# Kernel optimization log

Hardware: AMD Instinct MI355X
Metric: run time of the kernel (lower is better)

## Reference

```python
import jax, jax.numpy as jnp
import numpy as np

KS = 3          # kernel_size
NK = KS * KS    # sample points per output pixel
PAD = KS // 2   # 'same' zero padding


def setup_inputs() -> dict:
    key = jax.random.key(0)
    k1, k2, k3, k4 = jax.random.split(key, 4)
    B, H, W, C, F = 8, 64, 64, 128, 256
    x = jax.random.normal(k1, (B, H, W, C), jnp.float32)
    offset = jax.random.normal(k2, (B, H, W, 2 * NK), jnp.float32)
    modulation = jax.random.uniform(k3, (B, H, W, NK), jnp.float32)
    conv_kernel = jax.random.normal(k4, (KS, KS, C, F), jnp.float32) * 0.02
    conv_bias = jnp.zeros((F,), jnp.float32)
    return {"x": x, "offset": offset, "modulation": modulation,
            "conv_kernel": conv_kernel, "conv_bias": conv_bias}


def reference(x, offset, modulation, conv_kernel, conv_bias):
    B, H, W, C = x.shape
    # zero pad ('same')
    xp = jnp.pad(x, ((0, 0), (PAD, PAD), (PAD, PAD), (0, 0)))
    ih, iw = H + 2 * PAD, W + 2 * PAD

    # offset: first NK channels are y-offsets, last NK are x-offsets -> [B,H,W,NK,2]
    off = jnp.stack([offset[..., :NK], offset[..., NK:]], axis=-1)

    # pixel centers in padded coords (start at 1 due to padding), stride 1
    gy, gx = jnp.meshgrid(jnp.arange(1, H + 1), jnp.arange(1, W + 1), indexing="ij")
    pix = jnp.stack([gy, gx], -1).reshape(1, H, W, 1, 2).astype(x.dtype)

    # kernel tap offsets, ky varies slowest after flatten (matches TF source)
    ky, kx = jnp.meshgrid(jnp.arange(-PAD, KS - PAD), jnp.arange(-PAD, KS - PAD), indexing="ij")
    ker = jnp.stack([ky.reshape(-1), kx.reshape(-1)], -1).reshape(1, 1, 1, NK, 2).astype(x.dtype)

    p = off + pix + ker                       # [B,H,W,NK,2] sampling locations
    y0f = jnp.floor(p[..., 0])
    x0f = jnp.floor(p[..., 1])
    y0 = jnp.clip(y0f, 0, ih - 1)
    x0 = jnp.clip(x0f, 0, iw - 1)
    y1 = jnp.clip(y0f + 1.0, 0, ih - 1)
    x1 = jnp.clip(x0f + 1.0, 0, iw - 1)

    bidx = jnp.arange(B).reshape(B, 1, 1, 1)

    def gather(yi, xi):  # -> [B,H,W,NK,C]
        return xp[bidx, yi.astype(jnp.int32), xi.astype(jnp.int32)]

    f00 = gather(y0, x0)
    f01 = gather(y1, x0)
    f10 = gather(y0, x1)
    f11 = gather(y1, x1)

    py = jnp.clip(p[..., 0], 0, ih - 1)[..., None]
    px = jnp.clip(p[..., 1], 0, iw - 1)[..., None]
    ly = py - y0[..., None]
    lx = px - x0[..., None]

    feats = ((1.0 - ly) * (1.0 - lx) * f00 + (1.0 - ly) * lx * f01
             + ly * (1.0 - lx) * f10 + ly * lx * f11)      # [B,H,W,NK,C]
    feats = feats * modulation[..., None]

    # rearrange exactly as the TF code: concat kernel-row chunks along H, then reshape
    feats = jnp.concatenate([feats[:, :, :, s:s + KS, :] for s in range(0, NK, KS)], axis=1)
    feats = feats.reshape(B, H * KS, W * KS, C)

    out = jax.lax.conv_general_dilated(
        feats, conv_kernel, window_strides=(KS, KS), padding="VALID",
        dimension_numbers=("NHWC", "HWIO", "NHWC"))
    return out + conv_bias
```

## Files before the change

### kernel.cpp

```cpp
#include <hip/hip_runtime.h>

typedef __attribute__((ext_vector_type(8))) short short8;
typedef __attribute__((ext_vector_type(4))) float f32x4;

__device__ __forceinline__ unsigned short f2bf(float f) {
  union { float f; unsigned u; } v; v.f = f;
  unsigned r = v.u + 0x7FFFu + ((v.u >> 16) & 1u);
  return (unsigned short)(r >> 16);
}

__device__ __forceinline__ short8 pack8(f32x4 a, f32x4 b) {
  short8 p;
  p[0] = (short)f2bf(a.x); p[1] = (short)f2bf(a.y);
  p[2] = (short)f2bf(a.z); p[3] = (short)f2bf(a.w);
  p[4] = (short)f2bf(b.x); p[5] = (short)f2bf(b.y);
  p[6] = (short)f2bf(b.z); p[7] = (short)f2bf(b.w);
  return p;
}

__device__ __forceinline__ short8 packEO(f32x4 e, f32x4 o) {
  short8 p;
  p[0] = (short)f2bf(e.x); p[1] = (short)f2bf(o.x);
  p[2] = (short)f2bf(e.y); p[3] = (short)f2bf(o.y);
  p[4] = (short)f2bf(e.z); p[5] = (short)f2bf(o.z);
  p[6] = (short)f2bf(e.w); p[7] = (short)f2bf(o.w);
  return p;
}

constexpr int KKt = 1152;
constexpr int Ff  = 256;
constexpr size_t WT_BYTES = (size_t)KKt * Ff * 2;
constexpr size_t XB_BYTES = (size_t)8 * 64 * 64 * 128 * 2;

__global__ void wt_prep(const float* __restrict__ kf, unsigned short* __restrict__ wtB) {
  int idx = blockIdx.x * 256 + threadIdx.x;
  int j  = idx & 7;
  int fr = (idx >> 3) & 15;
  int kg = (idx >> 7) & 3;
  int ft = (idx >> 9) & 15;
  int ks = (idx >> 13) & 3;
  int ch = idx >> 15;
  int k = ch * 128 + ks * 32 + kg * 8 + j;
  int f = ft * 16 + fr;
  wtB[idx] = f2bf(kf[k * Ff + f]);
}

__global__ void x_prep(const float* __restrict__ x, unsigned short* __restrict__ xb) {
  int i = (blockIdx.x * 512 + threadIdx.x) * 8;
  const f32x4* p = (const f32x4*)(x + i);
  *(short8*)(xb + i) = pack8(p[0], p[1]);
}

__global__ __launch_bounds__(1024, 8) void dcn_bf16(
    const unsigned short* __restrict__ xb, const float* __restrict__ off,
    const float* __restrict__ mo, const unsigned short* __restrict__ wtB,
    const float* __restrict__ bias, float* __restrict__ out) {
  __shared__ __align__(16) char At[2][64 * 272];

  const int b  = blockIdx.x & 7;
  const int oh = blockIdx.x >> 3;
  const int t  = threadIdx.x;
  const int lane = t & 63;
  const int wv   = t >> 6;
  const int mh   = wv & 1;
  const int fq   = wv >> 1;
  const int fr   = lane & 15;
  const int kg   = lane >> 4;
  const int sow  = t >> 4;
  const int c8   = t & 15;

  f32x4 acc[2][2];
#pragma unroll
  for (int i = 0; i < 2; ++i) { acc[i][0] = f32x4{0,0,0,0}; acc[i][1] = f32x4{0,0,0,0}; }

  float oyr[2], oxr[2], mmr[2];
  int   og[4]; float wg[4];

  auto loadOff = [&](int ch, int sl) {
    const int dy = ch / 3, dxk = ch - dy * 3;
    const int r = 3 * oh + dy, hp = r & 63, kp = ((r >> 6) * 3) + dxk;
    const int pix = (b * 64 + hp) * 64 + sow;
    oyr[sl] = off[pix * 18 + kp];
    oxr[sl] = off[pix * 18 + 9 + kp];
    mmr[sl] = mo[pix * 9 + kp];
  };

  auto calcW = [&](int ch, int sl) {
    const int dy = ch / 3, dxk = ch - dy * 3;
    const int r = 3 * oh + dy, hp = r & 63, kp = ((r >> 6) * 3) + dxk;
    const float py = oyr[sl] + (float)(hp + kp / 3);
    const float px = oxr[sl] + (float)(sow + kp % 3);
    const float mm = mmr[sl];
    const float y0f = floorf(py), x0f = floorf(px);
    const float y0 = fminf(fmaxf(y0f, 0.f), 65.f);
    const float y1 = fminf(fmaxf(y0f + 1.f, 0.f), 65.f);
    const float x0 = fminf(fmaxf(x0f, 0.f), 65.f);
    const float x1 = fminf(fmaxf(x0f + 1.f, 0.f), 65.f);
    const float ly = fminf(fmaxf(py, 0.f), 65.f) - y0;
    const float lx = fminf(fmaxf(px, 0.f), 65.f) - x0;
    wg[0] = (1.f - ly) * (1.f - lx) * mm;
    wg[1] = (1.f - ly) * lx * mm;
    wg[2] = ly * (1.f - lx) * mm;
    wg[3] = ly * lx * mm;
    const int iy0 = (int)y0, iy1 = (int)y1, ix0 = (int)x0, ix1 = (int)x1;
    const int yy[4] = {iy0, iy1, iy0, iy1};
    const int xx[4] = {ix0, ix0, ix1, ix1};
#pragma unroll
    for (int j = 0; j < 4; ++j) {
      const bool v = (yy[j] >= 1) & (yy[j] <= 64) & (xx[j] >= 1) & (xx[j] <= 64);
      int o = ((b * 64 + yy[j] - 1) * 64 + (xx[j] - 1)) * 128 + c8 * 8;
      if (!v) { o = 0; wg[j] = 0.f; }
      og[j] = o;
    }
  };

  auto ldQ = [&](int c) -> short8 {
    return *(const short8*)(xb + og[c]);
  };
  auto accQ = [&](short8 s, float w, f32x4& Pe, f32x4& Po) {
    union { short8 s; unsigned u[4]; } v; v.s = s;
#pragma unroll
    for (int i = 0; i < 4; ++i) {
      union { unsigned u; float f; } e, o;
      e.u = v.u[i] << 16;
      o.u = v.u[i] & 0xffff0000u;
      Pe[i] = fmaf(w, e.f, Pe[i]);
      Po[i] = fmaf(w, o.f, Po[i]);
    }
  };

  auto mmah = [&](int buf, int ch, int ks) {
    const unsigned short* bp = wtB + (((ch * 4 + ks) * 16 + fq * 2) * 64 + lane) * 8;
    short8 bf0 = *(const short8*)bp;
    short8 bf1 = *(const short8*)(bp + 512);
    short8 af[2];
#pragma unroll
    for (int m2 = 0; m2 < 2; ++m2)
      af[m2] = *(const short8*)(At[buf] + (mh * 32 + m2 * 16 + fr) * 272 + ks * 64 + kg * 16);
#pragma unroll
    for (int m2 = 0; m2 < 2; ++m2) {
      acc[m2][0] = __builtin_amdgcn_mfma_f32_16x16x32_bf16(af[m2], bf0, acc[m2][0], 0, 0, 0);
      acc[m2][1] = __builtin_amdgcn_mfma_f32_16x16x32_bf16(af[m2], bf1, acc[m2][1], 0, 0, 0);
    }
  };

  const int wb = sow * 272 + c8 * 16;

  loadOff(0, 0); loadOff(1, 1);
  calcW(0, 0);
  {
    short8 q0 = ldQ(0), q1 = ldQ(1), q2 = ldQ(2), q3 = ldQ(3);
    f32x4 Pe{0,0,0,0}, Po{0,0,0,0};
    accQ(q0, wg[0], Pe, Po); accQ(q1, wg[1], Pe, Po);
    accQ(q2, wg[2], Pe, Po); accQ(q3, wg[3], Pe, Po);
    *(short8*)(At[0] + wb) = packEO(Pe, Po);
  }
  __syncthreads();

#pragma unroll
  for (int ch = 0; ch < 9; ++ch) {
    const int buf = ch & 1;
    const bool hv = ch < 8;
    short8 q0, q1, q2, q3;
    f32x4 Pe{0,0,0,0}, Po{0,0,0,0};
    if (hv) {
      calcW(ch + 1, (ch + 1) & 1);
      q0 = ldQ(0); q1 = ldQ(1);
    }
    mmah(buf, ch, 0);
    if (hv) {
      q2 = ldQ(2); q3 = ldQ(3);
      accQ(q0, wg[0], Pe, Po);
    }
    mmah(buf, ch, 1);
    if (hv) accQ(q1, wg[1], Pe, Po);
    if (ch < 7) loadOff(ch + 2, ch & 1);
    mmah(buf, ch, 2);
    if (hv) {
      accQ(q2, wg[2], Pe, Po);
      accQ(q3, wg[3], Pe, Po);
      *(short8*)(At[buf ^ 1] + wb) = packEO(Pe, Po);
    }
    mmah(buf, ch, 3);
    __syncthreads();
  }

  float bs[2];
#pragma unroll
  for (int nb = 0; nb < 2; ++nb) bs[nb] = bias[fq * 32 + nb * 16 + fr];
  float* orow = out + (long)(b * 64 + oh) * 64 * 256;
#pragma unroll
  for (int m2 = 0; m2 < 2; ++m2) {
#pragma unroll
    for (int j = 0; j < 4; ++j) {
      const int row = mh * 32 + m2 * 16 + kg * 4 + j;
#pragma unroll
      for (int nb = 0; nb < 2; ++nb)
        orow[row * 256 + fq * 32 + nb * 16 + fr] = acc[m2][nb][j] + bs[nb];
    }
  }
}

__global__ __launch_bounds__(512, 4) void dcn_f32(
    const float* __restrict__ x, const float* __restrict__ off,
    const float* __restrict__ mo, const unsigned short* __restrict__ wtB,
    const float* __restrict__ bias, float* __restrict__ out) {
  __shared__ __align__(16) char At[2][64 * 272];
  const int b  = blockIdx.x & 7;
  const int oh = blockIdx.x >> 3;
  const int t  = threadIdx.x;
  const int lane = t & 63;
  const int wv   = t >> 6;
  const int fr   = lane & 15;
  const int kg   = lane >> 4;
  const int sow  = t >> 3;
  const int c16  = t & 7;

  f32x4 acc[4][2];
#pragma unroll
  for (int i = 0; i < 4; ++i) { acc[i][0] = f32x4{0,0,0,0}; acc[i][1] = f32x4{0,0,0,0}; }
  float oyr[2], oxr[2], mmr[2];
  int   og[4]; float wg[4];

  auto loadOff = [&](int ch, int sl) {
    const int dy = ch / 3, dxk = ch - dy * 3;
    const int r = 3 * oh + dy, hp = r & 63, kp = ((r >> 6) * 3) + dxk;
    const int pix = (b * 64 + hp) * 64 + sow;
    oyr[sl] = off[pix * 18 + kp];
    oxr[sl] = off[pix * 18 + 9 + kp];
    mmr[sl] = mo[pix * 9 + kp];
  };
  auto calcW = [&](int ch, int sl) {
    const int dy = ch / 3, dxk = ch - dy * 3;
    const int r = 3 * oh + dy, hp = r & 63, kp = ((r >> 6) * 3) + dxk;
    const float py = oyr[sl] + (float)(hp + kp / 3);
    const float px = oxr[sl] + (float)(sow + kp % 3);
    const float mm = mmr[sl];
    const float y0f = floorf(py), x0f = floorf(px);
    const float y0 = fminf(fmaxf(y0f, 0.f), 65.f);
    const float y1 = fminf(fmaxf(y0f + 1.f, 0.f), 65.f);
    const float x0 = fminf(fmaxf(x0f, 0.f), 65.f);
    const float x1 = fminf(fmaxf(x0f + 1.f, 0.f), 65.f);
    const float ly = fminf(fmaxf(py, 0.f), 65.f) - y0;
    const float lx = fminf(fmaxf(px, 0.f), 65.f) - x0;
    wg[0] = (1.f - ly) * (1.f - lx) * mm;
    wg[1] = (1.f - ly) * lx * mm;
    wg[2] = ly * (1.f - lx) * mm;
    wg[3] = ly * lx * mm;
    const int iy0 = (int)y0, iy1 = (int)y1, ix0 = (int)x0, ix1 = (int)x1;
    const int yy[4] = {iy0, iy1, iy0, iy1};
    const int xx[4] = {ix0, ix0, ix1, ix1};
#pragma unroll
    for (int j = 0; j < 4; ++j) {
      const bool v = (yy[j] >= 1) & (yy[j] <= 64) & (xx[j] >= 1) & (xx[j] <= 64);
      int o = ((b * 64 + yy[j] - 1) * 64 + (xx[j] - 1)) * 128 + c16 * 16;
      if (!v) { o = 0; wg[j] = 0.f; }
      og[j] = o;
    }
  };
  auto ldB = [&](int ch, int ks, short8* bf) {
    const unsigned short* p = wtB + (((ch * 4 + ks) * 16 + wv * 2) * 64 + lane) * 8;
    bf[0] = *(const short8*)p;
    bf[1] = *(const short8*)(p + 512);
  };
  auto mmah = [&](int buf, int ks, const short8* bf) {
    short8 af[4];
#pragma unroll
    for (int m2 = 0; m2 < 4; ++m2)
      af[m2] = *(const short8*)(At[buf] + (m2 * 16 + fr) * 272 + ks * 64 + kg * 16);
#pragma unroll
    for (int m2 = 0; m2 < 4; ++m2)
#pragma unroll
      for (int nb = 0; nb < 2; ++nb)
        acc[m2][nb] = __builtin_amdgcn_mfma_f32_16x16x32_bf16(af[m2], bf[nb], acc[m2][nb], 0, 0, 0);
  };
  auto ldC = [&](int c, f32x4* G) {
    const f32x4* p = (const f32x4*)(x + og[c]);
    G[0] = p[0]; G[1] = p[1]; G[2] = p[2]; G[3] = p[3];
  };
  const int wb = sow * 272 + c16 * 32;
  loadOff(0, 0); loadOff(1, 1);
  calcW(0, 0);
  {
    f32x4 G0[4], G1[4];
    ldC(0, G0); ldC(1, G1);
    f32x4 P0 = wg[0]*G0[0] + wg[1]*G1[0], P1 = wg[0]*G0[1] + wg[1]*G1[1];
    f32x4 P2 = wg[0]*G0[2] + wg[1]*G1[2], P3 = wg[0]*G0[3] + wg[1]*G1[3];
    ldC(2, G0); ldC(3, G1);
    P0 += wg[2]*G0[0] + wg[3]*G1[0]; P1 += wg[2]*G0[1] + wg[3]*G1[1];
    P2 += wg[2]*G0[2] + wg[3]*G1[2]; P3 += wg[2]*G0[3] + wg[3]*G1[3];
    *(short8*)(At[0] + wb)      = pack8(P0, P1);
    *(short8*)(At[0] + wb + 16) = pack8(P2, P3);
  }
  __syncthreads();
#pragma unroll
  for (int ch = 0; ch < 9; ++ch) {
    const int buf = ch & 1;
    const bool hv = ch < 8;
    if (hv) calcW(ch + 1, (ch + 1) & 1);
    short8 bA[2], bB[2];
    f32x4 G0[4], G1[4], P0, P1, P2, P3;
    ldB(ch, 0, bA);
    if (hv) ldC(0, G0);
    ldB(ch, 1, bB);
    mmah(buf, 0, bA);
    if (hv) { P0 = wg[0]*G0[0]; P1 = wg[0]*G0[1]; P2 = wg[0]*G0[2]; P3 = wg[0]*G0[3]; }
    if (hv) ldC(1, G1);
    ldB(ch, 2, bA);
    mmah(buf, 1, bB);
    if (hv) { P0 += wg[1]*G1[0]; P1 += wg[1]*G1[1]; P2 += wg[1]*G1[2]; P3 += wg[1]*G1[3]; }
    if (hv) ldC(2, G0);
    ldB(ch, 3, bB);
    if (ch < 7) loadOff(ch + 2, ch & 1);
    mmah(buf, 2, bA);
    if (hv) { P0 += wg[2]*G0[0]; P1 += wg[2]*G0[1]; P2 += wg[2]*G0[2]; P3 += wg[2]*G0[3]; }
    if (hv) ldC(3, G1);
    mmah(buf, 3, bB);
    if (hv) {
      P0 += wg[3]*G1[0]; P1 += wg[3]*G1[1]; P2 += wg[3]*G1[2]; P3 += wg[3]*G1[3];
      *(short8*)(At[buf ^ 1] + wb)      = pack8(P0, P1);
      *(short8*)(At[buf ^ 1] + wb + 16) = pack8(P2, P3);
    }
    __syncthreads();
  }
  float bs[2];
#pragma unroll
  for (int nb = 0; nb < 2; ++nb) bs[nb] = bias[wv * 32 + nb * 16 + fr];
  float* orow = out + (long)(b * 64 + oh) * 64 * 256;
#pragma unroll
  for (int m2 = 0; m2 < 4; ++m2) {
#pragma unroll
    for (int j = 0; j < 4; ++j) {
      const int ow = m2 * 16 + kg * 4 + j;
#pragma unroll
      for (int nb = 0; nb < 2; ++nb)
        orow[ow * 256 + wv * 32 + nb * 16 + fr] = acc[m2][nb][j] + bs[nb];
    }
  }
}

extern "C" void kernel_launch(void* const* d_in, const int* in_sizes, int n_in,
                              void* d_out, int out_size, void* d_ws, size_t ws_size,
                              hipStream_t stream) {
  const float* x    = (const float*)d_in[0];
  const float* off  = (const float*)d_in[1];
  const float* mo   = (const float*)d_in[2];
  const float* kf   = (const float*)d_in[3];
  const float* bias = (const float*)d_in[4];
  float* outp = (float*)d_out;
  unsigned short* wtB = (unsigned short*)d_ws;

  wt_prep<<<1152, 256, 0, stream>>>(kf, wtB);
  if (ws_size >= WT_BYTES + XB_BYTES) {
    unsigned short* xb = (unsigned short*)((char*)d_ws + WT_BYTES);
    x_prep<<<1024, 512, 0, stream>>>(x, xb);
    dcn_bf16<<<512, 1024, 0, stream>>>(xb, off, mo, wtB, bias, outp);
  } else {
    dcn_f32<<<512, 512, 0, stream>>>(x, off, mo, wtB, bias, outp);
  }
}
```

Baseline: 57.05 us.

## Split DCN kernel into producer/consumer warps and merge prep kernels

The fused bf16 kernel is restructured into warp specialization. Eight wavefronts now gather and bilinearly blend the sampled features into double-buffered LDS, each handling 16 channels per pixel. The other eight run the MFMA GEMM over all 64 output columns, with s_setprio raised to favor matrix work. The two prep kernels (x to bf16 conversion and weight reshuffle) are merged into one launch to save a launch. The split halves the number of threads doing gathers and doubles the per-wave MFMA work, and occupancy hints drop from 8 to 4.

```diff
diff --git a/kernel.cpp b/kernel.cpp
--- a/kernel.cpp
+++ b/kernel.cpp
@@ -32,26 +32,29 @@
 constexpr size_t WT_BYTES = (size_t)KKt * Ff * 2;
 constexpr size_t XB_BYTES = (size_t)8 * 64 * 64 * 128 * 2;
 
-__global__ void wt_prep(const float* __restrict__ kf, unsigned short* __restrict__ wtB) {
-  int idx = blockIdx.x * 256 + threadIdx.x;
-  int j  = idx & 7;
-  int fr = (idx >> 3) & 15;
-  int kg = (idx >> 7) & 3;
-  int ft = (idx >> 9) & 15;
-  int ks = (idx >> 13) & 3;
-  int ch = idx >> 15;
-  int k = ch * 128 + ks * 32 + kg * 8 + j;
-  int f = ft * 16 + fr;
-  wtB[idx] = f2bf(kf[k * Ff + f]);
-}
-
-__global__ void x_prep(const float* __restrict__ x, unsigned short* __restrict__ xb) {
-  int i = (blockIdx.x * 512 + threadIdx.x) * 8;
-  const f32x4* p = (const f32x4*)(x + i);
-  *(short8*)(xb + i) = pack8(p[0], p[1]);
-}
-
-__global__ __launch_bounds__(1024, 8) void dcn_bf16(
+__global__ __launch_bounds__(256) void prep_small(
+    const float* __restrict__ x, const float* __restrict__ kf,
+    unsigned short* __restrict__ xb, unsigned short* __restrict__ wtB) {
+  const int bid = blockIdx.x;
+  if (bid < 2048) {
+    int i = (bid * 256 + threadIdx.x) * 8;
+    const f32x4* p = (const f32x4*)(x + i);
+    *(short8*)(xb + i) = pack8(p[0], p[1]);
+  } else {
+    int idx = (bid - 2048) * 256 + threadIdx.x;
+    int j  = idx & 7;
+    int fr = (idx >> 3) & 15;
+    int kg = (idx >> 7) & 3;
+    int ft = (idx >> 9) & 15;
+    int ks = (idx >> 13) & 3;
+    int ch = idx >> 15;
+    int k = ch * 128 + ks * 32 + kg * 8 + j;
+    int f = ft * 16 + fr;
+    wtB[idx] = f2bf(kf[k * Ff + f]);
+  }
+}
+
+__global__ __launch_bounds__(1024, 4) void dcn_spec(
     const unsigned short* __restrict__ xb, const float* __restrict__ off,
     const float* __restrict__ mo, const unsigned short* __restrict__ wtB,
     const float* __restrict__ bias, float* __restrict__ out) {
@@ -60,143 +63,141 @@
   const int b  = blockIdx.x & 7;
   const int oh = blockIdx.x >> 3;
   const int t  = threadIdx.x;
-  const int lane = t & 63;
-  const int wv   = t >> 6;
-  const int mh   = wv & 1;
-  const int fq   = wv >> 1;
-  const int fr   = lane & 15;
-  const int kg   = lane >> 4;
-  const int sow  = t >> 4;
-  const int c8   = t & 15;
-
-  f32x4 acc[2][2];
-#pragma unroll
-  for (int i = 0; i < 2; ++i) { acc[i][0] = f32x4{0,0,0,0}; acc[i][1] = f32x4{0,0,0,0}; }
-
-  float oyr[2], oxr[2], mmr[2];
-  int   og[4]; float wg[4];
-
-  auto loadOff = [&](int ch, int sl) {
-    const int dy = ch / 3, dxk = ch - dy * 3;
-    const int r = 3 * oh + dy, hp = r & 63, kp = ((r >> 6) * 3) + dxk;
-    const int pix = (b * 64 + hp) * 64 + sow;
-    oyr[sl] = off[pix * 18 + kp];
-    oxr[sl] = off[pix * 18 + 9 + kp];
-    mmr[sl] = mo[pix * 9 + kp];
-  };
-
-  auto calcW = [&](int ch, int sl) {
-    const int dy = ch / 3, dxk = ch - dy * 3;
-    const int r = 3 * oh + dy, hp = r & 63, kp = ((r >> 6) * 3) + dxk;
-    const float py = oyr[sl] + (float)(hp + kp / 3);
-    const float px = oxr[sl] + (float)(sow + kp % 3);
-    const float mm = mmr[sl];
-    const float y0f = floorf(py), x0f = floorf(px);
-    const float y0 = fminf(fmaxf(y0f, 0.f), 65.f);
-    const float y1 = fminf(fmaxf(y0f + 1.f, 0.f), 65.f);
-    const float x0 = fminf(fmaxf(x0f, 0.f), 65.f);
-    const float x1 = fminf(fmaxf(x0f + 1.f, 0.f), 65.f);
-    const float ly = fminf(fmaxf(py, 0.f), 65.f) - y0;
-    const float lx = fminf(fmaxf(px, 0.f), 65.f) - x0;
-    wg[0] = (1.f - ly) * (1.f - lx) * mm;
-    wg[1] = (1.f - ly) * lx * mm;
-    wg[2] = ly * (1.f - lx) * mm;
-    wg[3] = ly * lx * mm;
-    const int iy0 = (int)y0, iy1 = (int)y1, ix0 = (int)x0, ix1 = (int)x1;
-    const int yy[4] = {iy0, iy1, iy0, iy1};
-    const int xx[4] = {ix0, ix0, ix1, ix1};
-#pragma unroll
-    for (int j = 0; j < 4; ++j) {
-      const bool v = (yy[j] >= 1) & (yy[j] <= 64) & (xx[j] >= 1) & (xx[j] <= 64);
-      int o = ((b * 64 + yy[j] - 1) * 64 + (xx[j] - 1)) * 128 + c8 * 8;
-      if (!v) { o = 0; wg[j] = 0.f; }
-      og[j] = o;
-    }
-  };
-
-  auto ldQ = [&](int c) -> short8 {
-    return *(const short8*)(xb + og[c]);
-  };
-  auto accQ = [&](short8 s, float w, f32x4& Pe, f32x4& Po) {
-    union { short8 s; unsigned u[4]; } v; v.s = s;
-#pragma unroll
-    for (int i = 0; i < 4; ++i) {
-      union { unsigned u; float f; } e, o;
-      e.u = v.u[i] << 16;
-      o.u = v.u[i] & 0xffff0000u;
-      Pe[i] = fmaf(w, e.f, Pe[i]);
-      Po[i] = fmaf(w, o.f, Po[i]);
-    }
-  };
-
-  auto mmah = [&](int buf, int ch, int ks) {
-    const unsigned short* bp = wtB + (((ch * 4 + ks) * 16 + fq * 2) * 64 + lane) * 8;
-    short8 bf0 = *(const short8*)bp;
-    short8 bf1 = *(const short8*)(bp + 512);
-    short8 af[2];
-#pragma unroll
-    for (int m2 = 0; m2 < 2; ++m2)
-      af[m2] = *(const short8*)(At[buf] + (mh * 32 + m2 * 16 + fr) * 272 + ks * 64 + kg * 16);
-#pragma unroll
-    for (int m2 = 0; m2 < 2; ++m2) {
-      acc[m2][0] = __builtin_amdgcn_mfma_f32_16x16x32_bf16(af[m2], bf0, acc[m2][0], 0, 0, 0);
-      acc[m2][1] = __builtin_amdgcn_mfma_f32_16x16x32_bf16(af[m2], bf1, acc[m2][1], 0, 0, 0);
-    }
-  };
-
-  const int wb = sow * 272 + c8 * 16;
-
-  loadOff(0, 0); loadOff(1, 1);
-  calcW(0, 0);
-  {
-    short8 q0 = ldQ(0), q1 = ldQ(1), q2 = ldQ(2), q3 = ldQ(3);
-    f32x4 Pe{0,0,0,0}, Po{0,0,0,0};
-    accQ(q0, wg[0], Pe, Po); accQ(q1, wg[1], Pe, Po);
-    accQ(q2, wg[2], Pe, Po); accQ(q3, wg[3], Pe, Po);
-    *(short8*)(At[0] + wb) = packEO(Pe, Po);
-  }
-  __syncthreads();
-
-#pragma unroll
-  for (int ch = 0; ch < 9; ++ch) {
-    const int buf = ch & 1;
-    const bool hv = ch < 8;
-    short8 q0, q1, q2, q3;
-    f32x4 Pe{0,0,0,0}, Po{0,0,0,0};
-    if (hv) {
-      calcW(ch + 1, (ch + 1) & 1);
-      q0 = ldQ(0); q1 = ldQ(1);
-    }
-    mmah(buf, ch, 0);
-    if (hv) {
-      q2 = ldQ(2); q3 = ldQ(3);
-      accQ(q0, wg[0], Pe, Po);
-    }
-    mmah(buf, ch, 1);
-    if (hv) accQ(q1, wg[1], Pe, Po);
-    if (ch < 7) loadOff(ch + 2, ch & 1);
-    mmah(buf, ch, 2);
-    if (hv) {
-      accQ(q2, wg[2], Pe, Po);
-      accQ(q3, wg[3], Pe, Po);
-      *(short8*)(At[buf ^ 1] + wb) = packEO(Pe, Po);
-    }
-    mmah(buf, ch, 3);
+
+  if (t >= 512) {
+    const int pt  = t - 512;
+    const int sow = pt >> 3;
+    const int c16 = pt & 7;
+    const int wb  = sow * 272 + c16 * 32;
+    float oyr[2], oxr[2], mmr[2];
+    int og[4]; float wg[4];
+
+    auto loadOff = [&](int ch, int sl) {
+      const int dy = ch / 3, dxk = ch - dy * 3;
+      const int r = 3 * oh + dy, hp = r & 63, kp = ((r >> 6) * 3) + dxk;
+      const int pix = (b * 64 + hp) * 64 + sow;
+      oyr[sl] = off[pix * 18 + kp];
+      oxr[sl] = off[pix * 18 + 9 + kp];
+      mmr[sl] = mo[pix * 9 + kp];
+    };
+    auto calcW = [&](int ch, int sl) {
+      const int dy = ch / 3, dxk = ch - dy * 3;
+      const int r = 3 * oh + dy, hp = r & 63, kp = ((r >> 6) * 3) + dxk;
+      const float py = oyr[sl] + (float)(hp + kp / 3);
+      const float px = oxr[sl] + (float)(sow + kp % 3);
+      const float mm = mmr[sl];
+      const float y0f = floorf(py), x0f = floorf(px);
+      const float y0 = fminf(fmaxf(y0f, 0.f), 65.f);
+      const float y1 = fminf(fmaxf(y0f + 1.f, 0.f), 65.f);
+      const float x0 = fminf(fmaxf(x0f, 0.f), 65.f);
+      const float x1 = fminf(fmaxf(x0f + 1.f, 0.f), 65.f);
+      const float ly = fminf(fmaxf(py, 0.f), 65.f) - y0;
+      const float lx = fminf(fmaxf(px, 0.f), 65.f) - x0;
+      wg[0] = (1.f - ly) * (1.f - lx) * mm;
+      wg[1] = (1.f - ly) * lx * mm;
+      wg[2] = ly * (1.f - lx) * mm;
+      wg[3] = ly * lx * mm;
+      const int iy0 = (int)y0, iy1 = (int)y1, ix0 = (int)x0, ix1 = (int)x1;
+      const int yy[4] = {iy0, iy1, iy0, iy1};
+      const int xx[4] = {ix0, ix0, ix1, ix1};
+#pragma unroll
+      for (int j = 0; j < 4; ++j) {
+        const bool v = (yy[j] >= 1) & (yy[j] <= 64) & (xx[j] >= 1) & (xx[j] <= 64);
+        int o = ((b * 64 + yy[j] - 1) * 64 + (xx[j] - 1)) * 128 + c16 * 16;
+        if (!v) { o = 0; wg[j] = 0.f; }
+        og[j] = o;
+      }
+    };
+    auto accQ = [&](short8 s, float w, f32x4& Pe, f32x4& Po) {
+      union { short8 s; unsigned u[4]; } v; v.s = s;
+#pragma unroll
+      for (int i = 0; i < 4; ++i) {
+        union { unsigned u; float f; } e, o;
+        e.u = v.u[i] << 16;
+        o.u = v.u[i] & 0xffff0000u;
+        Pe[i] = fmaf(w, e.f, Pe[i]);
+        Po[i] = fmaf(w, o.f, Po[i]);
+      }
+    };
+    auto pstage = [&](int ch, int sl, char* dst) {
+      calcW(ch, sl);
+      const short8* p0 = (const short8*)(xb + og[0]);
+      const short8* p1 = (const short8*)(xb + og[1]);
+      const short8* p2 = (const short8*)(xb + og[2]);
+      const short8* p3 = (const short8*)(xb + og[3]);
+      short8 a0 = p0[0], a1 = p0[1];
+      short8 b0 = p1[0], b1 = p1[1];
+      short8 c0 = p2[0], c1 = p2[1];
+      short8 d0 = p3[0], d1 = p3[1];
+      f32x4 Pe0{0,0,0,0}, Po0{0,0,0,0}, Pe1{0,0,0,0}, Po1{0,0,0,0};
+      accQ(a0, wg[0], Pe0, Po0); accQ(a1, wg[0], Pe1, Po1);
+      accQ(b0, wg[1], Pe0, Po0); accQ(b1, wg[1], Pe1, Po1);
+      accQ(c0, wg[2], Pe0, Po0); accQ(c1, wg[2], Pe1, Po1);
+      accQ(d0, wg[3], Pe0, Po0); accQ(d1, wg[3], Pe1, Po1);
+      *(short8*)(dst + wb)      = packEO(Pe0, Po0);
+      *(short8*)(dst + wb + 16) = packEO(Pe1, Po1);
+    };
+
+    loadOff(0, 0);
+    loadOff(1, 1);
+    pstage(0, 0, At[0]);
     __syncthreads();
-  }
-
-  float bs[2];
-#pragma unroll
-  for (int nb = 0; nb < 2; ++nb) bs[nb] = bias[fq * 32 + nb * 16 + fr];
-  float* orow = out + (long)(b * 64 + oh) * 64 * 256;
-#pragma unroll
-  for (int m2 = 0; m2 < 2; ++m2) {
-#pragma unroll
-    for (int j = 0; j < 4; ++j) {
-      const int row = mh * 32 + m2 * 16 + kg * 4 + j;
-#pragma unroll
-      for (int nb = 0; nb < 2; ++nb)
-        orow[row * 256 + fq * 32 + nb * 16 + fr] = acc[m2][nb][j] + bs[nb];
+#pragma unroll
+    for (int ch = 0; ch < 9; ++ch) {
+      if (ch < 8) {
+        if (ch < 7) loadOff(ch + 2, ch & 1);
+        pstage(ch + 1, (ch + 1) & 1, At[(ch + 1) & 1]);
+      }
+      __syncthreads();
+    }
+  } else {
+    const int lane = t & 63;
+    const int fq   = t >> 6;
+    const int fr   = lane & 15;
+    const int kg   = lane >> 4;
+
+    f32x4 acc[4][2];
+#pragma unroll
+    for (int i = 0; i < 4; ++i) { acc[i][0] = f32x4{0,0,0,0}; acc[i][1] = f32x4{0,0,0,0}; }
+
+    auto compute = [&](int buf, int ch) {
+      __builtin_amdgcn_s_setprio(1);
+#pragma unroll
+      for (int ks = 0; ks < 4; ++ks) {
+        const unsigned short* bp = wtB + (((ch * 4 + ks) * 16 + fq * 2) * 64 + lane) * 8;
+        short8 bf0 = *(const short8*)bp;
+        short8 bf1 = *(const short8*)(bp + 512);
+        short8 af[4];
+#pragma unroll
+        for (int m2 = 0; m2 < 4; ++m2)
+          af[m2] = *(const short8*)(At[buf] + (m2 * 16 + fr) * 272 + ks * 64 + kg * 16);
+#pragma unroll
+        for (int m2 = 0; m2 < 4; ++m2) {
+          acc[m2][0] = __builtin_amdgcn_mfma_f32_16x16x32_bf16(af[m2], bf0, acc[m2][0], 0, 0, 0);
+          acc[m2][1] = __builtin_amdgcn_mfma_f32_16x16x32_bf16(af[m2], bf1, acc[m2][1], 0, 0, 0);
+        }
+      }
+      __builtin_amdgcn_s_setprio(0);
+    };
+
+    __syncthreads();
+#pragma unroll
+    for (int ch = 0; ch < 9; ++ch) {
+      compute(ch & 1, ch);
+      __syncthreads();
+    }
+
+    const float bs0 = bias[fq * 32 + fr];
+    const float bs1 = bias[fq * 32 + 16 + fr];
+    float* orow = out + (long)(b * 64 + oh) * 64 * 256;
+#pragma unroll
+    for (int m2 = 0; m2 < 4; ++m2) {
+#pragma unroll
+      for (int j = 0; j < 4; ++j) {
+        const int ow = m2 * 16 + kg * 4 + j;
+        orow[ow * 256 + fq * 32 + fr]      = acc[m2][0][j] + bs0;
+        orow[ow * 256 + fq * 32 + 16 + fr] = acc[m2][1][j] + bs1;
+      }
     }
   }
 }
@@ -339,6 +340,19 @@
   }
 }
 
+__global__ void wt_prep_only(const float* __restrict__ kf, unsigned short* __restrict__ wtB) {
+  int idx = blockIdx.x * 256 + threadIdx.x;
+  int j  = idx & 7;
+  int fr = (idx >> 3) & 15;
+  int kg = (idx >> 7) & 3;
+  int ft = (idx >> 9) & 15;
+  int ks = (idx >> 13) & 3;
+  int ch = idx >> 15;
+  int k = ch * 128 + ks * 32 + kg * 8 + j;
+  int f = ft * 16 + fr;
+  wtB[idx] = f2bf(kf[k * Ff + f]);
+}
+
 extern "C" void kernel_launch(void* const* d_in, const int* in_sizes, int n_in,
                               void* d_out, int out_size, void* d_ws, size_t ws_size,
                               hipStream_t stream) {
@@ -350,12 +364,12 @@
   float* outp = (float*)d_out;
   unsigned short* wtB = (unsigned short*)d_ws;
 
-  wt_prep<<<1152, 256, 0, stream>>>(kf, wtB);
   if (ws_size >= WT_BYTES + XB_BYTES) {
     unsigned short* xb = (unsigned short*)((char*)d_ws + WT_BYTES);
-    x_prep<<<1024, 512, 0, stream>>>(x, xb);
-    dcn_bf16<<<512, 1024, 0, stream>>>(xb, off, mo, wtB, bias, outp);
+    prep_small<<<3200, 256, 0, stream>>>(x, kf, xb, wtB);
+    dcn_spec<<<512, 1024, 0, stream>>>(xb, off, mo, wtB, bias, outp);
   } else {
+    wt_prep_only<<<1152, 256, 0, stream>>>(kf, wtB);
     dcn_f32<<<512, 512, 0, stream>>>(x, off, mo, wtB, bias, outp);
   }
 }
```

Measured after the change: 51.82 us. -9.2%, faster.

## Split each output row into two 32-pixel blocks and merge prep kernels

Applied to the files above, without the earlier changes.

The main bf16 kernel now gives each block 32 output pixels instead of 64. That doubles the grid to 1024 blocks of 512 threads, and each wave computes one 16-row M tile against four 16-column N tiles. The aim is better load balance and occupancy across CUs, at the cost of each block re-reading the full weight slice for half as many pixels. Separately, the x-to-bf16 and weight-to-bf16 prep kernels are merged into one launch to cut per-launch overhead.

```diff
diff --git a/kernel.cpp b/kernel.cpp
--- a/kernel.cpp
+++ b/kernel.cpp
@@ -32,33 +32,38 @@
 constexpr size_t WT_BYTES = (size_t)KKt * Ff * 2;
 constexpr size_t XB_BYTES = (size_t)8 * 64 * 64 * 128 * 2;
 
-__global__ void wt_prep(const float* __restrict__ kf, unsigned short* __restrict__ wtB) {
-  int idx = blockIdx.x * 256 + threadIdx.x;
-  int j  = idx & 7;
-  int fr = (idx >> 3) & 15;
-  int kg = (idx >> 7) & 3;
-  int ft = (idx >> 9) & 15;
-  int ks = (idx >> 13) & 3;
-  int ch = idx >> 15;
-  int k = ch * 128 + ks * 32 + kg * 8 + j;
-  int f = ft * 16 + fr;
-  wtB[idx] = f2bf(kf[k * Ff + f]);
-}
-
-__global__ void x_prep(const float* __restrict__ x, unsigned short* __restrict__ xb) {
-  int i = (blockIdx.x * 512 + threadIdx.x) * 8;
-  const f32x4* p = (const f32x4*)(x + i);
-  *(short8*)(xb + i) = pack8(p[0], p[1]);
-}
-
-__global__ __launch_bounds__(1024, 8) void dcn_bf16(
+__global__ __launch_bounds__(256) void prep_small(
+    const float* __restrict__ x, const float* __restrict__ kf,
+    unsigned short* __restrict__ xb, unsigned short* __restrict__ wtB) {
+  const int bid = blockIdx.x;
+  if (bid < 2048) {
+    int i = (bid * 256 + threadIdx.x) * 8;
+    const f32x4* p = (const f32x4*)(x + i);
+    *(short8*)(xb + i) = pack8(p[0], p[1]);
+  } else {
+    int idx = (bid - 2048) * 256 + threadIdx.x;
+    int j  = idx & 7;
+    int fr = (idx >> 3) & 15;
+    int kg = (idx >> 7) & 3;
+    int ft = (idx >> 9) & 15;
+    int ks = (idx >> 13) & 3;
+    int ch = idx >> 15;
+    int k = ch * 128 + ks * 32 + kg * 8 + j;
+    int f = ft * 16 + fr;
+    wtB[idx] = f2bf(kf[k * Ff + f]);
+  }
+}
+
+__global__ __launch_bounds__(512, 8) void dcn_m32(
     const unsigned short* __restrict__ xb, const float* __restrict__ off,
     const float* __restrict__ mo, const unsigned short* __restrict__ wtB,
     const float* __restrict__ bias, float* __restrict__ out) {
-  __shared__ __align__(16) char At[2][64 * 272];
-
-  const int b  = blockIdx.x & 7;
-  const int oh = blockIdx.x >> 3;
+  __shared__ __align__(16) char At[2][32 * 272];
+
+  const int b    = blockIdx.x & 7;
+  const int q    = blockIdx.x >> 3;
+  const int oh   = q >> 1;
+  const int mseg = q & 1;
   const int t  = threadIdx.x;
   const int lane = t & 63;
   const int wv   = t >> 6;
@@ -69,27 +74,27 @@
   const int sow  = t >> 4;
   const int c8   = t & 15;
 
-  f32x4 acc[2][2];
-#pragma unroll
-  for (int i = 0; i < 2; ++i) { acc[i][0] = f32x4{0,0,0,0}; acc[i][1] = f32x4{0,0,0,0}; }
+  f32x4 acc[4];
+#pragma unroll
+  for (int i = 0; i < 4; ++i) acc[i] = f32x4{0.f, 0.f, 0.f, 0.f};
 
   float oyr[2], oxr[2], mmr[2];
   int   og[4]; float wg[4];
+  const int ow = mseg * 32 + sow;
 
   auto loadOff = [&](int ch, int sl) {
     const int dy = ch / 3, dxk = ch - dy * 3;
     const int r = 3 * oh + dy, hp = r & 63, kp = ((r >> 6) * 3) + dxk;
-    const int pix = (b * 64 + hp) * 64 + sow;
+    const int pix = (b * 64 + hp) * 64 + ow;
     oyr[sl] = off[pix * 18 + kp];
     oxr[sl] = off[pix * 18 + 9 + kp];
     mmr[sl] = mo[pix * 9 + kp];
   };
-
   auto calcW = [&](int ch, int sl) {
     const int dy = ch / 3, dxk = ch - dy * 3;
     const int r = 3 * oh + dy, hp = r & 63, kp = ((r >> 6) * 3) + dxk;
     const float py = oyr[sl] + (float)(hp + kp / 3);
-    const float px = oxr[sl] + (float)(sow + kp % 3);
+    const float px = oxr[sl] + (float)(ow + kp % 3);
     const float mm = mmr[sl];
     const float y0f = floorf(py), x0f = floorf(px);
     const float y0 = fminf(fmaxf(y0f, 0.f), 65.f);
@@ -113,10 +118,7 @@
       og[j] = o;
     }
   };
-
-  auto ldQ = [&](int c) -> short8 {
-    return *(const short8*)(xb + og[c]);
-  };
+  auto ldQ = [&](int c) -> short8 { return *(const short8*)(xb + og[c]); };
   auto accQ = [&](short8 s, float w, f32x4& Pe, f32x4& Po) {
     union { short8 s; unsigned u[4]; } v; v.s = s;
 #pragma unroll
@@ -128,19 +130,14 @@
       Po[i] = fmaf(w, o.f, Po[i]);
     }
   };
-
   auto mmah = [&](int buf, int ch, int ks) {
-    const unsigned short* bp = wtB + (((ch * 4 + ks) * 16 + fq * 2) * 64 + lane) * 8;
-    short8 bf0 = *(const short8*)bp;
-    short8 bf1 = *(const short8*)(bp + 512);
-    short8 af[2];
-#pragma unroll
-    for (int m2 = 0; m2 < 2; ++m2)
-      af[m2] = *(const short8*)(At[buf] + (mh * 32 + m2 * 16 + fr) * 272 + ks * 64 + kg * 16);
-#pragma unroll
-    for (int m2 = 0; m2 < 2; ++m2) {
-      acc[m2][0] = __builtin_amdgcn_mfma_f32_16x16x32_bf16(af[m2], bf0, acc[m2][0], 0, 0, 0);
-      acc[m2][1] = __builtin_amdgcn_mfma_f32_16x16x32_bf16(af[m2], bf1, acc[m2][1], 0, 0, 0);
+    short8 af = *(const short8*)(At[buf] + (mh * 16 + fr) * 272 + ks * 64 + kg * 16);
+    const unsigned short* bp =
+        wtB + ((((ch * 4 + ks) * 16 + fq * 4) * 64 + lane) << 3);
+#pragma unroll
+    for (int nb = 0; nb < 4; ++nb) {
+      short8 bf = *(const short8*)(bp + (nb << 9));
+      acc[nb] = __builtin_amdgcn_mfma_f32_16x16x32_bf16(af, bf, acc[nb], 0, 0, 0);
     }
   };
 
@@ -185,19 +182,16 @@
     __syncthreads();
   }
 
-  float bs[2];
-#pragma unroll
-  for (int nb = 0; nb < 2; ++nb) bs[nb] = bias[fq * 32 + nb * 16 + fr];
-  float* orow = out + (long)(b * 64 + oh) * 64 * 256;
-#pragma unroll
-  for (int m2 = 0; m2 < 2; ++m2) {
-#pragma unroll
-    for (int j = 0; j < 4; ++j) {
-      const int row = mh * 32 + m2 * 16 + kg * 4 + j;
-#pragma unroll
-      for (int nb = 0; nb < 2; ++nb)
-        orow[row * 256 + fq * 32 + nb * 16 + fr] = acc[m2][nb][j] + bs[nb];
-    }
+  float bs[4];
+#pragma unroll
+  for (int nb = 0; nb < 4; ++nb) bs[nb] = bias[fq * 64 + nb * 16 + fr];
+  float* orow = out + ((long)(b * 64 + oh) * 64 + mseg * 32) * 256;
+#pragma unroll
+  for (int j = 0; j < 4; ++j) {
+    const int row = mh * 16 + kg * 4 + j;
+#pragma unroll
+    for (int nb = 0; nb < 4; ++nb)
+      orow[row * 256 + fq * 64 + nb * 16 + fr] = acc[nb][j] + bs[nb];
   }
 }
 
@@ -339,6 +333,19 @@
   }
 }
 
+__global__ void wt_prep_only(const float* __restrict__ kf, unsigned short* __restrict__ wtB) {
+  int idx = blockIdx.x * 256 + threadIdx.x;
+  int j  = idx & 7;
+  int fr = (idx >> 3) & 15;
+  int kg = (idx >> 7) & 3;
+  int ft = (idx >> 9) & 15;
+  int ks = (idx >> 13) & 3;
+  int ch = idx >> 15;
+  int k = ch * 128 + ks * 32 + kg * 8 + j;
+  int f = ft * 16 + fr;
+  wtB[idx] = f2bf(kf[k * Ff + f]);
+}
+
 extern "C" void kernel_launch(void* const* d_in, const int* in_sizes, int n_in,
                               void* d_out, int out_size, void* d_ws, size_t ws_size,
                               hipStream_t stream) {
@@ -350,12 +357,12 @@
   float* outp = (float*)d_out;
   unsigned short* wtB = (unsigned short*)d_ws;
 
-  wt_prep<<<1152, 256, 0, stream>>>(kf, wtB);
   if (ws_size >= WT_BYTES + XB_BYTES) {
     unsigned short* xb = (unsigned short*)((char*)d_ws + WT_BYTES);
-    x_prep<<<1024, 512, 0, stream>>>(x, xb);
-    dcn_bf16<<<512, 1024, 0, stream>>>(xb, off, mo, wtB, bias, outp);
+    prep_small<<<3200, 256, 0, stream>>>(x, kf, xb, wtB);
+    dcn_m32<<<1024, 512, 0, stream>>>(xb, off, mo, wtB, bias, outp);
   } else {
+    wt_prep_only<<<1152, 256, 0, stream>>>(kf, wtB);
     dcn_f32<<<512, 512, 0, stream>>>(x, off, mo, wtB, bias, outp);
   }
 }
```

Result: slower. 74.52 us (+30.6%).
